# Optimization experiments

Measured on AMD Instinct MI355X. Metric: run time of the kernel, lower is better.

Reference implementation:

```python
import jax, jax.numpy as jnp
import numpy as np

FRACS = (0.25, 0.5, 0.25)  # per-expert top-fraction kept, from the original forward


def setup_inputs() -> dict:
    key = jax.random.key(0)
    ks = jax.random.split(key, 10)
    B, S, D, P, E, C = 1, 65536, 1024, 512, 3, 2
    s = 0.02
    return {
        "hidden_states": jax.random.normal(ks[0], (B, S, D), jnp.float32),
        "W_t1": jax.random.normal(ks[1], (D, P), jnp.float32) * s,   # TransMIL stand-in proj
        "W_cls1": jax.random.normal(ks[2], (P, C), jnp.float32) * s, # trans1 bag classifier
        "Wg0": jax.random.normal(ks[3], (P, 2), jnp.float32) * s,    # gate
        "Wg1": jax.random.normal(ks[4], (P, 2), jnp.float32) * s,    # gate1
        "Wg2": jax.random.normal(ks[5], (P, 2), jnp.float32) * s,    # gate2
        "W_clf": jax.random.normal(ks[6], (E, P, E), jnp.float32) * s,  # per-expert classifiers
        "W_a1": jax.random.normal(ks[7], (P, P), jnp.float32) * s,   # agg1 TransMIL stand-in proj
        "W_acls": jax.random.normal(ks[8], (P, C), jnp.float32) * s, # agg1 bag classifier
    }


def reference(hidden_states, W_t1, W_cls1, Wg0, Wg1, Wg2, W_clf, W_a1, W_acls):
    B, S, D = hidden_states.shape
    x = hidden_states.reshape(-1, D)               # (T, D) tokens
    T = x.shape[0]
    # trans1 (TransMIL stand-in): per-patch feature + mean-pool bag logits
    patches = jnp.tanh(x @ W_t1)                   # (T, P) patch_feature
    bag = patches.mean(0)
    Y_logits = (bag @ W_cls1)[None, :]             # (1, C)
    Y_prob = jax.nn.softmax(Y_logits, -1)
    Y_hat = jnp.argmax(Y_logits, -1)
    # three independent routers, softmax + top-1
    router_logits = patches @ Wg0                  # (T, 2)
    rw0 = jax.nn.softmax(router_logits.astype(jnp.float32), -1)
    w_top0 = rw0.max(-1)                           # top-1 routing weight (gate0) used as sort key for ALL experts
    sel0 = jnp.argmax(rw0, -1)
    sel1 = jnp.argmax(jax.nn.softmax((patches @ Wg1).astype(jnp.float32), -1), -1)
    sel2 = jnp.argmax(jax.nn.softmax((patches @ Wg2).astype(jnp.float32), -1), -1)
    masks = [sel0 == 1, sel1 == 1, sel2 == 1]      # expert_mask[e][1] token selection
    joint_losses = jnp.float32(0.0)
    sel_fs, nums_list = [], []
    for e in range(3):
        mask = masks[e]
        cnt = mask.sum().astype(jnp.int32)
        nums = jnp.floor(cnt.astype(jnp.float32) * FRACS[e]).astype(jnp.int32)
        nums = jnp.where(nums == 0, cnt, nums)     # 'if nums != 0 else all' branch
        key_ = jnp.where(mask, w_top0, -jnp.inf)
        order = jnp.argsort(-key_)                 # descending routing weight
        rank = jnp.zeros(T, jnp.int32).at[order].set(jnp.arange(T, dtype=jnp.int32))
        sel = mask & (rank < nums)                 # top-fraction tokens of this expert
        sel_f = sel.astype(patches.dtype)
        mean_feat = (patches * sel_f[:, None]).sum(0) / jnp.maximum(nums, 1).astype(patches.dtype)
        logits = mean_feat @ W_clf[e]              # (3,)
        if e < 2:                                  # CE loss only for experts 0,1
            joint_losses = joint_losses + (-jax.nn.log_softmax(logits)[e])
        sel_fs.append(sel_f)
        nums_list.append(nums)
    # agg1 (TransMIL stand-in) over concatenated represent_patchs == multiplicity-weighted mean
    feats2 = jnp.tanh(patches @ W_a1)              # (T, P)
    total_sel = sel_fs[0] + sel_fs[1] + sel_fs[2]
    total_n = (nums_list[0] + nums_list[1] + nums_list[2]).astype(patches.dtype)
    agg_bag = (feats2 * total_sel[:, None]).sum(0) / jnp.maximum(total_n, 1.0)
    e_Y_logits = (agg_bag @ W_acls)[None, :]
    e_Y_hat = jnp.argmax(e_Y_logits, -1)
    distribute = jnp.stack([jnp.asarray(T, jnp.int32), nums_list[0], nums_list[1], nums_list[2]])
    return (e_Y_logits, e_Y_hat, Y_logits, Y_prob, Y_hat, router_logits, joint_losses, distribute)
```

## Files before the change

### kernel.cpp

```cpp
#include <hip/hip_runtime.h>
#include <cstdint>
#include <cstddef>

#define T_TOK 65536
#define DDIM  1024
#define PDIM  512

typedef __attribute__((ext_vector_type(8))) short          shortx8;
typedef __attribute__((ext_vector_type(8))) unsigned short ushortx8;
typedef __attribute__((ext_vector_type(4))) float          floatx4;

__device__ __forceinline__ unsigned short f2bf_rn(float x){
  unsigned int u = __float_as_uint(x);
  unsigned int r = u + 0x7FFFu + ((u >> 16) & 1u);
  return (unsigned short)(r >> 16);
}
__device__ __forceinline__ float bf2f(unsigned short h){
  return __uint_as_float(((unsigned int)h) << 16);
}
__device__ __forceinline__ float ftanh(float x){
  float ez = __expf(2.f * x);
  return 1.f - 2.f / (ez + 1.f);
}

__global__ void prep(const float* __restrict__ Wt1, const float* __restrict__ Wa1,
                     unsigned short* __restrict__ W1th, unsigned short* __restrict__ W1tl,
                     unsigned short* __restrict__ Wath, unsigned short* __restrict__ Watl,
                     int* __restrict__ zbase)
{
  int gid = blockIdx.x * 256 + threadIdx.x;
  if (gid < 20544){ zbase[gid] = 0; return; }
  int i = gid - 20544;
  if (i < 524288){
    int p = i >> 10, k = i & 1023;
    float x = Wt1[(size_t)k * PDIM + p];
    unsigned short h = f2bf_rn(x);
    W1th[i] = h;
    W1tl[i] = f2bf_rn(x - bf2f(h));
    return;
  }
  i -= 524288;
  if (i < 262144){
    int n = i >> 9, k = i & 511;
    float x = Wa1[(size_t)k * PDIM + n];
    unsigned short h = f2bf_rn(x);
    Wath[i] = h;
    Watl[i] = f2bf_rn(x - bf2f(h));
  }
}

template<int MODE>
__global__ __launch_bounds__(256, 2)
void gemm_split(const float* __restrict__ A,
                const unsigned short* __restrict__ Bhg,
                const unsigned short* __restrict__ Blg,
                float* __restrict__ Cout,
                float* __restrict__ colacc,
                const int* __restrict__ cidx,
                const float* __restrict__ wgt,
                const int* __restrict__ params)
{
  constexpr int K = (MODE == 0) ? 1024 : 512;
  __shared__ unsigned short Ah[128][40];
  __shared__ unsigned short Al[128][40];
  __shared__ unsigned short Bh[128][40];
  __shared__ unsigned short Bl[128][40];
  __shared__ int   cidxl[128];
  __shared__ float wl[128];

  const int tid = threadIdx.x;
  const int m0 = blockIdx.y * 128;
  const int n0 = blockIdx.x * 128;

  if (MODE == 1){
    int count = params[21];
    if (m0 >= count) return;
    if (tid < 128){
      int g = m0 + tid;
      if (g < count){ cidxl[tid] = cidx[g]; wl[tid] = wgt[g]; }
      else          { cidxl[tid] = 0;       wl[tid] = 0.f;   }
    }
    __syncthreads();
  }

  const int lane = tid & 63;
  const int wv   = tid >> 6;
  const int wm   = (wv & 1) << 6;
  const int wn   = (wv >> 1) << 6;
  const int lr   = lane & 15;
  const int quad = lane >> 4;
  const int kb8  = quad << 3;

  floatx4 acc[4][4];
  #pragma unroll
  for (int i = 0; i < 4; i++)
    #pragma unroll
    for (int j = 0; j < 4; j++)
      acc[i][j] = (floatx4){0.f, 0.f, 0.f, 0.f};

  const int nkb = K >> 5;
  for (int kb = 0; kb < nkb; ++kb){
    const int k0 = kb << 5;
    #pragma unroll
    for (int i = 0; i < 4; i++){
      int lin = i * 256 + tid;
      int row = lin >> 3;
      int kq  = (lin & 7) << 2;
      size_t arow = (MODE == 0) ? (size_t)(m0 + row) : (size_t)cidxl[row];
      const float4 v = *(const float4*)(A + arow * K + k0 + kq);
      unsigned int ux = __float_as_uint(v.x), uy = __float_as_uint(v.y);
      unsigned int uz = __float_as_uint(v.z), uw = __float_as_uint(v.w);
      float rx = v.x - __uint_as_float(ux & 0xFFFF0000u);
      float ry = v.y - __uint_as_float(uy & 0xFFFF0000u);
      float rz = v.z - __uint_as_float(uz & 0xFFFF0000u);
      float rw = v.w - __uint_as_float(uw & 0xFFFF0000u);
      ushort4 h, l;
      h.x = (unsigned short)(ux >> 16); l.x = (unsigned short)(__float_as_uint(rx) >> 16);
      h.y = (unsigned short)(uy >> 16); l.y = (unsigned short)(__float_as_uint(ry) >> 16);
      h.z = (unsigned short)(uz >> 16); l.z = (unsigned short)(__float_as_uint(rz) >> 16);
      h.w = (unsigned short)(uw >> 16); l.w = (unsigned short)(__float_as_uint(rw) >> 16);
      *(ushort4*)&Ah[row][kq] = h;
      *(ushort4*)&Al[row][kq] = l;
    }
    #pragma unroll
    for (int i = 0; i < 2; i++){
      int lin = i * 256 + tid;
      int row = lin >> 2;
      int kq  = (lin & 3) << 3;
      size_t off = (size_t)(n0 + row) * K + k0 + kq;
      *(ushortx8*)&Bh[row][kq] = *(const ushortx8*)(Bhg + off);
      *(ushortx8*)&Bl[row][kq] = *(const ushortx8*)(Blg + off);
    }
    __syncthreads();
    shortx8 a0[4], a1[4], b0[4], b1[4];
    #pragma unroll
    for (int i = 0; i < 4; i++){
      a0[i] = *(const shortx8*)&Ah[wm + i * 16 + lr][kb8];
      a1[i] = *(const shortx8*)&Al[wm + i * 16 + lr][kb8];
      b0[i] = *(const shortx8*)&Bh[wn + i * 16 + lr][kb8];
      b1[i] = *(const shortx8*)&Bl[wn + i * 16 + lr][kb8];
    }
    #pragma unroll
    for (int i = 0; i < 4; i++){
      #pragma unroll
      for (int j = 0; j < 4; j++){
        acc[i][j] = __builtin_amdgcn_mfma_f32_16x16x32_bf16(a0[i], b0[j], acc[i][j], 0, 0, 0);
        acc[i][j] = __builtin_amdgcn_mfma_f32_16x16x32_bf16(a1[i], b0[j], acc[i][j], 0, 0, 0);
        acc[i][j] = __builtin_amdgcn_mfma_f32_16x16x32_bf16(a0[i], b1[j], acc[i][j], 0, 0, 0);
      }
    }
    __syncthreads();
  }

  float csum[4] = {0.f, 0.f, 0.f, 0.f};
  #pragma unroll
  for (int i = 0; i < 4; i++){
    float w0 = 1.f, w1 = 1.f, w2 = 1.f, w3 = 1.f;
    if (MODE == 1){
      const float4 wv4 = *(const float4*)&wl[wm + i * 16 + (quad << 2)];
      w0 = wv4.x; w1 = wv4.y; w2 = wv4.z; w3 = wv4.w;
    }
    #pragma unroll
    for (int j = 0; j < 4; j++){
      float t0 = ftanh(acc[i][j][0]);
      float t1 = ftanh(acc[i][j][1]);
      float t2 = ftanh(acc[i][j][2]);
      float t3 = ftanh(acc[i][j][3]);
      if (MODE == 0){
        size_t base = (size_t)(m0 + wm + i * 16 + (quad << 2)) * PDIM + (n0 + wn + j * 16 + lr);
        Cout[base]            = t0;
        Cout[base +     PDIM] = t1;
        Cout[base + 2 * PDIM] = t2;
        Cout[base + 3 * PDIM] = t3;
        csum[j] += t0 + t1 + t2 + t3;
      } else {
        csum[j] += t0 * w0 + t1 * w1 + t2 * w2 + t3 * w3;
      }
    }
  }
  #pragma unroll
  for (int j = 0; j < 4; j++){
    float s = csum[j];
    s += __shfl_xor(s, 16);
    s += __shfl_xor(s, 32);
    if (lane < 16) atomicAdd(&colacc[n0 + wn + j * 16 + lane], s);
  }
}

__global__ void gates_kernel(const float* __restrict__ patches,
                             const float* __restrict__ Wg0,
                             const float* __restrict__ Wg1,
                             const float* __restrict__ Wg2,
                             float* __restrict__ dout,
                             unsigned int* __restrict__ wkey,
                             unsigned char* __restrict__ mask3,
                             int* __restrict__ params,
                             int* __restrict__ hist)
{
  __shared__ int lc[3];
  const int tid = threadIdx.x;
  if (tid < 3) lc[tid] = 0;
  __syncthreads();
  const int lane = tid & 63;
  float wg[3][16];
  const float* Wgp[3] = {Wg0, Wg1, Wg2};
  #pragma unroll
  for (int g = 0; g < 3; g++){
    #pragma unroll
    for (int j = 0; j < 4; j++){
      float4 v = *(const float4*)(Wgp[g] + lane * 16 + j * 4);
      wg[g][j * 4 + 0] = v.x; wg[g][j * 4 + 1] = v.y;
      wg[g][j * 4 + 2] = v.z; wg[g][j * 4 + 3] = v.w;
    }
  }
  const int nw = gridDim.x << 2;
  for (int t = blockIdx.x * 4 + (tid >> 6); t < T_TOK; t += nw){
    const float* row = patches + (size_t)t * PDIM + lane * 8;
    float4 v0 = *(const float4*)row;
    float4 v1 = *(const float4*)(row + 4);
    float x[8] = {v0.x, v0.y, v0.z, v0.w, v1.x, v1.y, v1.z, v1.w};
    float g00 = 0, g01 = 0, g10 = 0, g11 = 0, g20 = 0, g21 = 0;
    #pragma unroll
    for (int j = 0; j < 8; j++){
      g00 += x[j] * wg[0][2 * j]; g01 += x[j] * wg[0][2 * j + 1];
      g10 += x[j] * wg[1][2 * j]; g11 += x[j] * wg[1][2 * j + 1];
      g20 += x[j] * wg[2][2 * j]; g21 += x[j] * wg[2][2 * j + 1];
    }
    #pragma unroll
    for (int off = 1; off < 64; off <<= 1){
      g00 += __shfl_xor(g00, off); g01 += __shfl_xor(g01, off);
      g10 += __shfl_xor(g10, off); g11 += __shfl_xor(g11, off);
      g20 += __shfl_xor(g20, off); g21 += __shfl_xor(g21, off);
    }
    if (lane == 0){
      dout[8 + 2 * t]     = g00;
      dout[8 + 2 * t + 1] = g01;
      int m0 = g01 > g00;
      int m1 = g11 > g10;
      int m2 = g21 > g20;
      mask3[t] = (unsigned char)(m0 | (m1 << 1) | (m2 << 2));
      float d = fabsf(g00 - g01);
      float w = 1.0f / (1.0f + __expf(-d));
      unsigned int u = __float_as_uint(w);
      u = u < 0x3F000000u ? 0x3F000000u : u;
      u = u > 0x3F7FFFFFu ? 0x3F7FFFFFu : u;
      wkey[t] = u;
      int b = (int)((u >> 11) & 0xFFFu);
      if (m0){ atomicAdd(&hist[b], 1);         atomicAdd(&lc[0], 1); }
      if (m1){ atomicAdd(&hist[4096 + b], 1);  atomicAdd(&lc[1], 1); }
      if (m2){ atomicAdd(&hist[8192 + b], 1);  atomicAdd(&lc[2], 1); }
    }
  }
  __syncthreads();
  if (tid < 3 && lc[tid]) atomicAdd(&params[tid], lc[tid]);
}

__global__ void find_bucket(int* __restrict__ params, const int* __restrict__ hist)
{
  __shared__ int cs[256], orig[256];
  __shared__ int selc, selrk;
  const int tid = threadIdx.x;
  for (int e = 0; e < 3; e++){
    int cnt = params[e];
    int shift = (e == 1) ? 1 : 2;
    int nums = cnt >> shift;
    if (nums == 0) nums = cnt;
    if (tid == 0) params[3 + e] = nums;
    __syncthreads();
    if (nums == 0){
      if (tid == 0){ params[6 + e] = -1; params[9 + e] = 0; }
      __syncthreads();
      continue;
    }
    const int* h = hist + e * 4096 + tid * 16;
    int s = 0;
    #pragma unroll
    for (int j = 0; j < 16; j++) s += h[j];
    cs[tid] = s; orig[tid] = s;
    __syncthreads();
    for (int off = 1; off < 256; off <<= 1){
      int v = (tid + off < 256) ? cs[tid + off] : 0;
      __syncthreads();
      cs[tid] += v;
      __syncthreads();
    }
    if (cs[tid] >= nums && (cs[tid] - orig[tid]) < nums){
      selc = tid; selrk = nums - (cs[tid] - orig[tid]);
    }
    __syncthreads();
    if (tid == 0){
      int ch = selc, rk = selrk;
      const int* hh = hist + e * 4096 + ch * 16;
      int acc = 0;
      for (int j = 15; j >= 0; j--){
        int c = hh[j];
        if (acc + c >= rk){ params[6 + e] = ch * 16 + j; params[9 + e] = rk - acc; break; }
        acc += c;
      }
    }
    __syncthreads();
  }
}

__global__ void level2hist(const int* __restrict__ params, const unsigned int* __restrict__ wkey,
                           const unsigned char* __restrict__ mask3, int* __restrict__ h2)
{
  const int e = blockIdx.y;
  const int B = params[6 + e];
  if (B < 0) return;
  const unsigned char bit = (unsigned char)(1u << e);
  const int t0 = blockIdx.x * 2048 + threadIdx.x;
  #pragma unroll
  for (int i = 0; i < 8; i++){
    int t = t0 + i * 256;
    if (mask3[t] & bit){
      unsigned int u = wkey[t];
      if ((int)((u >> 11) & 0xFFFu) == B) atomicAdd(&h2[e * 2048 + (u & 2047u)], 1);
    }
  }
}

__global__ void find_theta(int* __restrict__ params, const int* __restrict__ h2)
{
  const int e = blockIdx.x;
  const int tid = threadIdx.x;
  __shared__ int cs[256], orig[256];
  __shared__ int selc;
  int B = params[6 + e], rank = params[9 + e];
  if (B < 0){
    if (tid == 0){ params[12 + e] = (int)0xFFFFFFFFu; params[15 + e] = 0; params[18 + e] = 0; }
    return;
  }
  const int* h = h2 + e * 2048 + tid * 8;
  int s = 0;
  #pragma unroll
  for (int j = 0; j < 8; j++) s += h[j];
  cs[tid] = s; orig[tid] = s;
  __syncthreads();
  for (int off = 1; off < 256; off <<= 1){
    int v = (tid + off < 256) ? cs[tid + off] : 0;
    __syncthreads();
    cs[tid] += v;
    __syncthreads();
  }
  if (cs[tid] >= rank && (cs[tid] - orig[tid]) < rank) selc = tid;
  __syncthreads();
  if (tid == 0){
    int ch = selc;
    int rk = rank - (cs[ch] - orig[ch]);
    const int* hh = h2 + e * 2048 + ch * 8;
    int acc = 0;
    for (int j = 7; j >= 0; j--){
      int c = hh[j];
      if (acc + c >= rk){
        int sub = ch * 8 + j;
        params[12 + e] = (int)(0x3F000000u | ((unsigned)B << 11) | (unsigned)sub);
        params[15 + e] = rk - acc;
        params[18 + e] = c;
        break;
      }
      acc += c;
    }
  }
}

__global__ void mark_sel(const int* __restrict__ params, const unsigned int* __restrict__ wkey,
                         const unsigned char* __restrict__ mask3, unsigned char* __restrict__ selb)
{
  const int e = blockIdx.y;
  const int bx = blockIdx.x;
  const int tid = threadIdx.x;
  const unsigned int theta = (unsigned int)params[12 + e];
  const int r = params[15 + e];
  const int ceq = params[18 + e];
  const unsigned char bit = (unsigned char)(1u << e);
  unsigned char* sb = selb + e * T_TOK;
  if (ceq == r){
    int t0 = bx * 2048;
    #pragma unroll
    for (int i = 0; i < 8; i++){
      int t = t0 + i * 256 + tid;
      unsigned char mk = mask3[t] & bit;
      sb[t] = (mk && wkey[t] >= theta) ? 1 : 0;
    }
  } else {
    if (bx) return;
    __shared__ int basec;
    __shared__ int wsum[4];
    if (tid == 0) basec = 0;
    __syncthreads();
    const int lane = tid & 63, w = tid >> 6;
    for (int c = 0; c < 256; c++){
      int t = c * 256 + tid;
      unsigned char mk = mask3[t] & bit;
      unsigned int u = mk ? wkey[t] : 0u;
      bool gt = mk && (u > theta);
      bool eq = mk && (u == theta);
      unsigned long long bal = __ballot(eq);
      if (lane == 0) wsum[w] = __popcll(bal);
      __syncthreads();
      int wbase = 0;
      for (int ww = 0; ww < w; ww++) wbase += wsum[ww];
      int pos = basec + wbase + __popcll(bal & ((1ull << lane) - 1ull));
      sb[t] = (gt || (eq && pos < r)) ? 1 : 0;
      __syncthreads();
      if (tid == 0) basec += wsum[0] + wsum[1] + wsum[2] + wsum[3];
      __syncthreads();
    }
  }
}

__global__ void compact(const unsigned char* __restrict__ selb, int* __restrict__ cidx,
                        float* __restrict__ wgt, int* __restrict__ params)
{
  int t = blockIdx.x * 256 + threadIdx.x;
  int ts = selb[t] + selb[T_TOK + t] + selb[2 * T_TOK + t];
  int lane = threadIdx.x & 63;
  unsigned long long bal = __ballot(ts > 0);
  int base = 0;
  if (lane == 0) base = atomicAdd(&params[21], __popcll(bal));
  base = __shfl(base, 0);
  if (ts){
    int pos = base + __popcll(bal & ((1ull << lane) - 1ull));
    cidx[pos] = t;
    wgt[pos] = (float)ts;
  }
}

__global__ void meanfeat_c(const float* __restrict__ patches, const unsigned char* __restrict__ selb,
                           const int* __restrict__ cidx, const int* __restrict__ params,
                           float* __restrict__ mf)
{
  const int count = params[21];
  const int base = blockIdx.x * 256;
  if (base >= count) return;
  const int n = min(256, count - base);
  const int tid = threadIdx.x;
  __shared__ int cl[256];
  __shared__ unsigned char f0s[256], f1s[256];
  if (tid < n){
    int c = cidx[base + tid];
    cl[tid] = c;
    f0s[tid] = selb[c];
    f1s[tid] = selb[T_TOK + c];
  }
  __syncthreads();
  float s00 = 0, s01 = 0, s10 = 0, s11 = 0;
  for (int i = 0; i < n; i++){
    int f0 = f0s[i], f1 = f1s[i];
    if (f0 | f1){
      float2 v = *(const float2*)(patches + (size_t)cl[i] * PDIM + tid * 2);
      if (f0){ s00 += v.x; s01 += v.y; }
      if (f1){ s10 += v.x; s11 += v.y; }
    }
  }
  atomicAdd(&mf[tid * 2],       s00);
  atomicAdd(&mf[tid * 2 + 1],   s01);
  atomicAdd(&mf[512 + tid * 2],     s10);
  atomicAdd(&mf[512 + tid * 2 + 1], s11);
}

__global__ void finalize(const float* __restrict__ bagsum, const float* __restrict__ aggsum,
                         const float* __restrict__ mf, const int* __restrict__ params,
                         const float* __restrict__ Wcls1, const float* __restrict__ Wclf,
                         const float* __restrict__ Wacls, float* __restrict__ dout)
{
  const int lane = threadIdx.x;
  const int nums0 = params[3], nums1 = params[4], nums2 = params[5];
  const float invT = 1.0f / 65536.0f;
  const float inv0 = 1.0f / (float)(nums0 > 0 ? nums0 : 1);
  const float inv1 = 1.0f / (float)(nums1 > 0 ? nums1 : 1);
  const float totn = (float)(nums0 + nums1 + nums2);
  const float invA = 1.0f / fmaxf(totn, 1.0f);
  float y0 = 0, y1 = 0, a0 = 0, a1 = 0;
  float l00 = 0, l01 = 0, l02 = 0, l10 = 0, l11 = 0, l12 = 0;
  #pragma unroll
  for (int j = 0; j < 8; j++){
    int p = lane * 8 + j;
    float bg = bagsum[p] * invT;
    y0 += bg * Wcls1[p * 2]; y1 += bg * Wcls1[p * 2 + 1];
    float ag = aggsum[p] * invA;
    a0 += ag * Wacls[p * 2]; a1 += ag * Wacls[p * 2 + 1];
    float m0v = mf[p] * inv0;
    l00 += m0v * Wclf[p * 3]; l01 += m0v * Wclf[p * 3 + 1]; l02 += m0v * Wclf[p * 3 + 2];
    float m1v = mf[512 + p] * inv1;
    l10 += m1v * Wclf[1536 + p * 3]; l11 += m1v * Wclf[1536 + p * 3 + 1]; l12 += m1v * Wclf[1536 + p * 3 + 2];
  }
  #pragma unroll
  for (int off = 1; off < 64; off <<= 1){
    y0 += __shfl_xor(y0, off);   y1 += __shfl_xor(y1, off);
    a0 += __shfl_xor(a0, off);   a1 += __shfl_xor(a1, off);
    l00 += __shfl_xor(l00, off); l01 += __shfl_xor(l01, off); l02 += __shfl_xor(l02, off);
    l10 += __shfl_xor(l10, off); l11 += __shfl_xor(l11, off); l12 += __shfl_xor(l12, off);
  }
  if (lane == 0){
    dout[0] = a0; dout[1] = a1;
    dout[2] = (a1 > a0) ? 1.0f : 0.0f;
    dout[3] = y0; dout[4] = y1;
    float mx = fmaxf(y0, y1), e0 = expf(y0 - mx), e1 = expf(y1 - mx), inv = 1.0f / (e0 + e1);
    dout[5] = e0 * inv; dout[6] = e1 * inv;
    dout[7] = (y1 > y0) ? 1.0f : 0.0f;
    float m3 = fmaxf(fmaxf(l00, l01), l02);
    float lse0 = m3 + logf(expf(l00 - m3) + expf(l01 - m3) + expf(l02 - m3));
    float m4 = fmaxf(fmaxf(l10, l11), l12);
    float lse1 = m4 + logf(expf(l10 - m4) + expf(l11 - m4) + expf(l12 - m4));
    dout[131080] = (lse0 - l00) + (lse1 - l11);
    dout[131081] = 65536.0f;
    dout[131082] = (float)nums0;
    dout[131083] = (float)nums1;
    dout[131084] = (float)nums2;
  }
}

extern "C" void kernel_launch(void* const* d_in, const int* in_sizes, int n_in,
                              void* d_out, int out_size, void* d_ws, size_t ws_size,
                              hipStream_t stream)
{
  const float* X      = (const float*)d_in[0];
  const float* W_t1   = (const float*)d_in[1];
  const float* W_cls1 = (const float*)d_in[2];
  const float* Wg0    = (const float*)d_in[3];
  const float* Wg1    = (const float*)d_in[4];
  const float* Wg2    = (const float*)d_in[5];
  const float* W_clf  = (const float*)d_in[6];
  const float* W_a1   = (const float*)d_in[7];
  const float* W_acls = (const float*)d_in[8];
  float* dout = (float*)d_out;
  char* ws = (char*)d_ws;

  float*          patches = (float*)         (ws + 0);
  unsigned short* W1th    = (unsigned short*)(ws + 134217728);
  unsigned short* W1tl    = (unsigned short*)(ws + 135266304);
  unsigned short* Wath    = (unsigned short*)(ws + 136314880);
  unsigned short* Watl    = (unsigned short*)(ws + 136839168);
  unsigned int*   wkey    = (unsigned int*)  (ws + 137363456);
  unsigned char*  mask3   = (unsigned char*) (ws + 137625600);
  unsigned char*  selb    = (unsigned char*) (ws + 137691136);
  int*            cidx    = (int*)           (ws + 137887744);
  float*          wgt     = (float*)         (ws + 138149888);
  int*            zbase   = (int*)           (ws + 138412032);
  int*            hist    = zbase;
  int*            h2      = zbase + 12288;
  int*            params  = zbase + 18432;
  float*          bagsum  = (float*)(zbase + 18496);
  float*          aggsum  = (float*)(zbase + 19008);
  float*          mf      = (float*)(zbase + 19520);

  prep<<<3153, 256, 0, stream>>>(W_t1, W_a1, W1th, W1tl, Wath, Watl, zbase);

  gemm_split<0><<<dim3(4, 512), 256, 0, stream>>>(
      X, W1th, W1tl, patches, bagsum, nullptr, nullptr, nullptr);

  gates_kernel<<<512, 256, 0, stream>>>(
      patches, Wg0, Wg1, Wg2, dout, wkey, mask3, params, hist);

  find_bucket<<<1, 256, 0, stream>>>(params, hist);
  level2hist<<<dim3(32, 3), 256, 0, stream>>>(params, wkey, mask3, h2);
  find_theta<<<3, 256, 0, stream>>>(params, h2);
  mark_sel<<<dim3(32, 3), 256, 0, stream>>>(params, wkey, mask3, selb);
  compact<<<256, 256, 0, stream>>>(selb, cidx, wgt, params);

  meanfeat_c<<<256, 256, 0, stream>>>(patches, selb, cidx, params, mf);

  gemm_split<1><<<dim3(4, 512), 256, 0, stream>>>(
      patches, Wath, Watl, nullptr, aggsum, cidx, wgt, params);

  finalize<<<1, 64, 0, stream>>>(bagsum, aggsum, mf, params, W_cls1, W_clf, W_acls, dout);
}
```

Measured before the change: 732.6 us.

## Rewrite split-bf16 GEMM with 256x256 tiles, double-buffered LDS and direct-to-LDS weight loads

Both split-precision GEMMs now use 256x256 tiles with 512 threads, double-buffered LDS and direct global-to-LDS loads for the weights. The weights are pre-swizzled in prep into a tiled, XOR-permuted layout to avoid bank conflicts. The k-loop is split into four MFMA phases with explicit waitcnt, barriers and setprio so the next tile's loads overlap the current tile's compute, and mode 0 blocks are remapped for L2 locality. The larger tiles cut re-reads of A and B from global memory. In exchange the kernel uses more LDS and registers per block, and the hand-placed waits and barriers are fragile.

```diff
diff --git a/kernel.cpp b/kernel.cpp
--- a/kernel.cpp
+++ b/kernel.cpp
@@ -23,6 +23,34 @@
   return 1.f - 2.f / (ez + 1.f);
 }
 
+__device__ __forceinline__ void gload16(const void* g, void* l){
+  __builtin_amdgcn_global_load_lds(
+      (const __attribute__((address_space(1))) unsigned int*)g,
+      (__attribute__((address_space(3))) unsigned int*)l, 16, 0, 0);
+}
+__device__ __forceinline__ void bar(){
+  asm volatile("" ::: "memory");
+  __builtin_amdgcn_s_barrier();
+  asm volatile("" ::: "memory");
+}
+#define WAIT_VMC(n) asm volatile("s_waitcnt vmcnt(" #n ")" ::: "memory")
+#define WAIT_LGKM0  do { asm volatile("s_waitcnt lgkmcnt(0)" ::: "memory"); \
+                         __builtin_amdgcn_sched_barrier(0); } while(0)
+
+__device__ __forceinline__ void split2(const float4 a, const float4 b,
+                                       ushortx8* hi, ushortx8* lo){
+  float vs[8] = {a.x, a.y, a.z, a.w, b.x, b.y, b.z, b.w};
+  ushortx8 h, l;
+  #pragma unroll
+  for (int j = 0; j < 8; j++){
+    unsigned int u = __float_as_uint(vs[j]);
+    float r = vs[j] - __uint_as_float(u & 0xFFFF0000u);
+    h[j] = (unsigned short)(u >> 16);
+    l[j] = (unsigned short)(__float_as_uint(r) >> 16);
+  }
+  *hi = h; *lo = l;
+}
+
 __global__ void prep(const float* __restrict__ Wt1, const float* __restrict__ Wa1,
                      unsigned short* __restrict__ W1th, unsigned short* __restrict__ W1tl,
                      unsigned short* __restrict__ Wath, unsigned short* __restrict__ Watl,
@@ -32,8 +60,15 @@
   if (gid < 20544){ zbase[gid] = 0; return; }
   int i = gid - 20544;
   if (i < 524288){
-    int p = i >> 10, k = i & 1023;
-    float x = Wt1[(size_t)k * PDIM + p];
+    int e   = i & 7;
+    int g16 = i >> 3;
+    int s   = g16 & 3;
+    int row = (g16 >> 2) & 255;
+    int tb  = g16 >> 10;
+    int nb  = tb & 1, kt = tb >> 1;
+    int n = nb * 256 + row;
+    int k = kt * 32 + ((s ^ (row & 3)) << 3) + e;
+    float x = Wt1[(size_t)k * PDIM + n];
     unsigned short h = f2bf_rn(x);
     W1th[i] = h;
     W1tl[i] = f2bf_rn(x - bf2f(h));
@@ -41,7 +76,14 @@
   }
   i -= 524288;
   if (i < 262144){
-    int n = i >> 9, k = i & 511;
+    int e   = i & 7;
+    int g16 = i >> 3;
+    int s   = g16 & 3;
+    int row = (g16 >> 2) & 255;
+    int tb  = g16 >> 10;
+    int nb  = tb & 1, kt = tb >> 1;
+    int n = nb * 256 + row;
+    int k = kt * 32 + ((s ^ (row & 3)) << 3) + e;
     float x = Wa1[(size_t)k * PDIM + n];
     unsigned short h = f2bf_rn(x);
     Wath[i] = h;
@@ -50,7 +92,7 @@
 }
 
 template<int MODE>
-__global__ __launch_bounds__(256, 2)
+__global__ __launch_bounds__(512, 2)
 void gemm_split(const float* __restrict__ A,
                 const unsigned short* __restrict__ Bhg,
                 const unsigned short* __restrict__ Blg,
@@ -60,22 +102,26 @@
                 const float* __restrict__ wgt,
                 const int* __restrict__ params)
 {
-  constexpr int K = (MODE == 0) ? 1024 : 512;
-  __shared__ unsigned short Ah[128][40];
-  __shared__ unsigned short Al[128][40];
-  __shared__ unsigned short Bh[128][40];
-  __shared__ unsigned short Bl[128][40];
-  __shared__ int   cidxl[128];
-  __shared__ float wl[128];
+  constexpr int K  = (MODE == 0) ? 1024 : 512;
+  constexpr int NT = K >> 5;
+
+  __shared__ unsigned short AhL[2][8192];
+  __shared__ unsigned short AlL[2][8192];
+  __shared__ unsigned short BhL[2][8192];
+  __shared__ unsigned short BlL[2][8192];
+  __shared__ int   cidxl[256];
+  __shared__ float wl[256];
 
   const int tid = threadIdx.x;
-  const int m0 = blockIdx.y * 128;
-  const int n0 = blockIdx.x * 128;
+  const int d = blockIdx.x + (blockIdx.y << 1);
+  const int lin = (MODE == 0) ? (((d & 7) << 6) + (d >> 3)) : d;
+  const int bx = lin & 1, by = lin >> 1;
+  const int m0 = by << 8, n0 = bx << 8;
 
   if (MODE == 1){
-    int count = params[21];
+    const int count = params[21];
     if (m0 >= count) return;
-    if (tid < 128){
+    if (tid < 256){
       int g = m0 + tid;
       if (g < count){ cidxl[tid] = cidx[g]; wl[tid] = wgt[g]; }
       else          { cidxl[tid] = 0;       wl[tid] = 0.f;   }
@@ -85,105 +131,198 @@
 
   const int lane = tid & 63;
   const int wv   = tid >> 6;
-  const int wm   = (wv & 1) << 6;
-  const int wn   = (wv >> 1) << 6;
-  const int lr   = lane & 15;
-  const int quad = lane >> 4;
-  const int kb8  = quad << 3;
-
-  floatx4 acc[4][4];
-  #pragma unroll
-  for (int i = 0; i < 4; i++)
+  const int wm   = wv >> 2;
+  const int wn   = wv & 3;
+  const int lr   = lane & 15, quad = lane >> 4;
+  const int sq   = (quad ^ (lr & 3)) << 4;
+
+  const int abase = (wm * 128 + lr) * 64 + sq;
+  const int bbase = (wn * 64  + lr) * 64 + sq;
+
+  const int rowW = tid >> 1, half = tid & 1;
+  const size_t arowg = (MODE == 0) ? (size_t)(m0 + rowW) : (size_t)cidxl[rowW];
+  const float* ap = A + arowg * K + half * 16;
+  const int wb0 = rowW * 64 + ((( half * 2     ) ^ (rowW & 3)) << 4);
+  const int wb1 = rowW * 64 + ((( half * 2 + 1 ) ^ (rowW & 3)) << 4);
+
+  floatx4 acc[8][4];
+  #pragma unroll
+  for (int i = 0; i < 8; i++)
     #pragma unroll
     for (int j = 0; j < 4; j++)
       acc[i][j] = (floatx4){0.f, 0.f, 0.f, 0.f};
 
-  const int nkb = K >> 5;
-  for (int kb = 0; kb < nkb; ++kb){
-    const int k0 = kb << 5;
-    #pragma unroll
-    for (int i = 0; i < 4; i++){
-      int lin = i * 256 + tid;
-      int row = lin >> 3;
-      int kq  = (lin & 7) << 2;
-      size_t arow = (MODE == 0) ? (size_t)(m0 + row) : (size_t)cidxl[row];
-      const float4 v = *(const float4*)(A + arow * K + k0 + kq);
-      unsigned int ux = __float_as_uint(v.x), uy = __float_as_uint(v.y);
-      unsigned int uz = __float_as_uint(v.z), uw = __float_as_uint(v.w);
-      float rx = v.x - __uint_as_float(ux & 0xFFFF0000u);
-      float ry = v.y - __uint_as_float(uy & 0xFFFF0000u);
-      float rz = v.z - __uint_as_float(uz & 0xFFFF0000u);
-      float rw = v.w - __uint_as_float(uw & 0xFFFF0000u);
-      ushort4 h, l;
-      h.x = (unsigned short)(ux >> 16); l.x = (unsigned short)(__float_as_uint(rx) >> 16);
-      h.y = (unsigned short)(uy >> 16); l.y = (unsigned short)(__float_as_uint(ry) >> 16);
-      h.z = (unsigned short)(uz >> 16); l.z = (unsigned short)(__float_as_uint(rz) >> 16);
-      h.w = (unsigned short)(uw >> 16); l.w = (unsigned short)(__float_as_uint(rw) >> 16);
-      *(ushort4*)&Ah[row][kq] = h;
-      *(ushort4*)&Al[row][kq] = l;
-    }
-    #pragma unroll
-    for (int i = 0; i < 2; i++){
-      int lin = i * 256 + tid;
-      int row = lin >> 2;
-      int kq  = (lin & 3) << 3;
-      size_t off = (size_t)(n0 + row) * K + k0 + kq;
-      *(ushortx8*)&Bh[row][kq] = *(const ushortx8*)(Bhg + off);
-      *(ushortx8*)&Bl[row][kq] = *(const ushortx8*)(Blg + off);
-    }
-    __syncthreads();
-    shortx8 a0[4], a1[4], b0[4], b1[4];
-    #pragma unroll
-    for (int i = 0; i < 4; i++){
-      a0[i] = *(const shortx8*)&Ah[wm + i * 16 + lr][kb8];
-      a1[i] = *(const shortx8*)&Al[wm + i * 16 + lr][kb8];
-      b0[i] = *(const shortx8*)&Bh[wn + i * 16 + lr][kb8];
-      b1[i] = *(const shortx8*)&Bl[wn + i * 16 + lr][kb8];
-    }
-    #pragma unroll
-    for (int i = 0; i < 4; i++){
+  float4 av0, av1, av2, av3;
+
+  {
+    av0 = *(const float4*)(ap + 0);
+    av1 = *(const float4*)(ap + 4);
+    av2 = *(const float4*)(ap + 8);
+    av3 = *(const float4*)(ap + 12);
+    const size_t tb = (size_t)bx * 8192;
+    gload16(Bhg + tb + tid * 8,        (char*)BhL[0] + tid * 16);
+    gload16(Bhg + tb + 4096 + tid * 8, (char*)BhL[0] + 8192 + tid * 16);
+    gload16(Blg + tb + tid * 8,        (char*)BlL[0] + tid * 16);
+    gload16(Blg + tb + 4096 + tid * 8, (char*)BlL[0] + 8192 + tid * 16);
+    WAIT_VMC(4);
+    ushortx8 h, l;
+    split2(av0, av1, &h, &l);
+    *(ushortx8*)((char*)AhL[0] + wb0) = h;
+    *(ushortx8*)((char*)AlL[0] + wb0) = l;
+    split2(av2, av3, &h, &l);
+    *(ushortx8*)((char*)AhL[0] + wb1) = h;
+    *(ushortx8*)((char*)AlL[0] + wb1) = l;
+    WAIT_VMC(0);
+    asm volatile("s_waitcnt lgkmcnt(0)" ::: "memory");
+    bar();
+  }
+
+  #pragma unroll 2
+  for (int t = 0; t < NT; ++t){
+    const int cur = t & 1, nxt = cur ^ 1;
+    const int kn = (t + 1 < NT) ? (t + 1) : t;
+    const char* AhC = (const char*)AhL[cur];
+    const char* AlC = (const char*)AlL[cur];
+    const char* BhC = (const char*)BhL[cur];
+    const char* BlC = (const char*)BlL[cur];
+
+    shortx8 aH[4], aL[4], bH0[2], bL0[2], bH1[2], bL1[2];
+
+    #pragma unroll
+    for (int mt = 0; mt < 4; mt++){
+      aH[mt] = *(const shortx8*)(AhC + abase + mt * 1024);
+      aL[mt] = *(const shortx8*)(AlC + abase + mt * 1024);
+    }
+    #pragma unroll
+    for (int nt = 0; nt < 2; nt++){
+      bH0[nt] = *(const shortx8*)(BhC + bbase + nt * 1024);
+      bL0[nt] = *(const shortx8*)(BlC + bbase + nt * 1024);
+    }
+    {
+      const float* apk = ap + kn * 32;
+      av0 = *(const float4*)(apk);
+      av1 = *(const float4*)(apk + 4);
+      av2 = *(const float4*)(apk + 8);
+      av3 = *(const float4*)(apk + 12);
+    }
+    bar();
+    WAIT_LGKM0;
+    __builtin_amdgcn_s_setprio(1);
+    #pragma unroll
+    for (int mt = 0; mt < 4; mt++)
       #pragma unroll
-      for (int j = 0; j < 4; j++){
-        acc[i][j] = __builtin_amdgcn_mfma_f32_16x16x32_bf16(a0[i], b0[j], acc[i][j], 0, 0, 0);
-        acc[i][j] = __builtin_amdgcn_mfma_f32_16x16x32_bf16(a1[i], b0[j], acc[i][j], 0, 0, 0);
-        acc[i][j] = __builtin_amdgcn_mfma_f32_16x16x32_bf16(a0[i], b1[j], acc[i][j], 0, 0, 0);
+      for (int nt = 0; nt < 2; nt++){
+        acc[mt][nt] = __builtin_amdgcn_mfma_f32_16x16x32_bf16(aH[mt], bH0[nt], acc[mt][nt], 0, 0, 0);
+        acc[mt][nt] = __builtin_amdgcn_mfma_f32_16x16x32_bf16(aL[mt], bH0[nt], acc[mt][nt], 0, 0, 0);
+        acc[mt][nt] = __builtin_amdgcn_mfma_f32_16x16x32_bf16(aH[mt], bL0[nt], acc[mt][nt], 0, 0, 0);
       }
-    }
-    __syncthreads();
+    __builtin_amdgcn_s_setprio(0);
+    bar();
+
+    #pragma unroll
+    for (int nt = 0; nt < 2; nt++){
+      bH1[nt] = *(const shortx8*)(BhC + bbase + (2 + nt) * 1024);
+      bL1[nt] = *(const shortx8*)(BlC + bbase + (2 + nt) * 1024);
+    }
+    {
+      const size_t tb = (size_t)(kn * 2 + bx) * 8192;
+      gload16(Bhg + tb + tid * 8,        (char*)BhL[nxt] + tid * 16);
+      gload16(Bhg + tb + 4096 + tid * 8, (char*)BhL[nxt] + 8192 + tid * 16);
+      gload16(Blg + tb + tid * 8,        (char*)BlL[nxt] + tid * 16);
+      gload16(Blg + tb + 4096 + tid * 8, (char*)BlL[nxt] + 8192 + tid * 16);
+    }
+    bar();
+    WAIT_LGKM0;
+    __builtin_amdgcn_s_setprio(1);
+    #pragma unroll
+    for (int mt = 0; mt < 4; mt++)
+      #pragma unroll
+      for (int nt = 0; nt < 2; nt++){
+        acc[mt][2 + nt] = __builtin_amdgcn_mfma_f32_16x16x32_bf16(aH[mt], bH1[nt], acc[mt][2 + nt], 0, 0, 0);
+        acc[mt][2 + nt] = __builtin_amdgcn_mfma_f32_16x16x32_bf16(aL[mt], bH1[nt], acc[mt][2 + nt], 0, 0, 0);
+        acc[mt][2 + nt] = __builtin_amdgcn_mfma_f32_16x16x32_bf16(aH[mt], bL1[nt], acc[mt][2 + nt], 0, 0, 0);
+      }
+    __builtin_amdgcn_s_setprio(0);
+    bar();
+
+    #pragma unroll
+    for (int mt = 0; mt < 4; mt++){
+      aH[mt] = *(const shortx8*)(AhC + abase + (4 + mt) * 1024);
+      aL[mt] = *(const shortx8*)(AlC + abase + (4 + mt) * 1024);
+    }
+    WAIT_VMC(4);
+    {
+      ushortx8 h, l;
+      split2(av0, av1, &h, &l);
+      *(ushortx8*)((char*)AhL[nxt] + wb0) = h;
+      *(ushortx8*)((char*)AlL[nxt] + wb0) = l;
+      split2(av2, av3, &h, &l);
+      *(ushortx8*)((char*)AhL[nxt] + wb1) = h;
+      *(ushortx8*)((char*)AlL[nxt] + wb1) = l;
+    }
+    bar();
+    WAIT_LGKM0;
+    __builtin_amdgcn_s_setprio(1);
+    #pragma unroll
+    for (int mt = 0; mt < 4; mt++)
+      #pragma unroll
+      for (int nt = 0; nt < 2; nt++){
+        acc[4 + mt][nt] = __builtin_amdgcn_mfma_f32_16x16x32_bf16(aH[mt], bH0[nt], acc[4 + mt][nt], 0, 0, 0);
+        acc[4 + mt][nt] = __builtin_amdgcn_mfma_f32_16x16x32_bf16(aL[mt], bH0[nt], acc[4 + mt][nt], 0, 0, 0);
+        acc[4 + mt][nt] = __builtin_amdgcn_mfma_f32_16x16x32_bf16(aH[mt], bL0[nt], acc[4 + mt][nt], 0, 0, 0);
+      }
+    __builtin_amdgcn_s_setprio(0);
+    bar();
+
+    WAIT_VMC(0);
+    bar();
+    WAIT_LGKM0;
+    __builtin_amdgcn_s_setprio(1);
+    #pragma unroll
+    for (int mt = 0; mt < 4; mt++)
+      #pragma unroll
+      for (int nt = 0; nt < 2; nt++){
+        acc[4 + mt][2 + nt] = __builtin_amdgcn_mfma_f32_16x16x32_bf16(aH[mt], bH1[nt], acc[4 + mt][2 + nt], 0, 0, 0);
+        acc[4 + mt][2 + nt] = __builtin_amdgcn_mfma_f32_16x16x32_bf16(aL[mt], bH1[nt], acc[4 + mt][2 + nt], 0, 0, 0);
+        acc[4 + mt][2 + nt] = __builtin_amdgcn_mfma_f32_16x16x32_bf16(aH[mt], bL1[nt], acc[4 + mt][2 + nt], 0, 0, 0);
+      }
+    __builtin_amdgcn_s_setprio(0);
+    bar();
   }
 
   float csum[4] = {0.f, 0.f, 0.f, 0.f};
   #pragma unroll
-  for (int i = 0; i < 4; i++){
+  for (int mt = 0; mt < 8; mt++){
     float w0 = 1.f, w1 = 1.f, w2 = 1.f, w3 = 1.f;
     if (MODE == 1){
-      const float4 wv4 = *(const float4*)&wl[wm + i * 16 + (quad << 2)];
+      const float4 wv4 = *(const float4*)&wl[wm * 128 + mt * 16 + (quad << 2)];
       w0 = wv4.x; w1 = wv4.y; w2 = wv4.z; w3 = wv4.w;
     }
     #pragma unroll
-    for (int j = 0; j < 4; j++){
-      float t0 = ftanh(acc[i][j][0]);
-      float t1 = ftanh(acc[i][j][1]);
-      float t2 = ftanh(acc[i][j][2]);
-      float t3 = ftanh(acc[i][j][3]);
+    for (int nt = 0; nt < 4; nt++){
+      float t0 = ftanh(acc[mt][nt][0]);
+      float t1 = ftanh(acc[mt][nt][1]);
+      float t2 = ftanh(acc[mt][nt][2]);
+      float t3 = ftanh(acc[mt][nt][3]);
       if (MODE == 0){
-        size_t base = (size_t)(m0 + wm + i * 16 + (quad << 2)) * PDIM + (n0 + wn + j * 16 + lr);
+        size_t base = (size_t)(m0 + wm * 128 + mt * 16 + (quad << 2)) * PDIM
+                    + (n0 + wn * 64 + nt * 16 + lr);
         Cout[base]            = t0;
         Cout[base +     PDIM] = t1;
         Cout[base + 2 * PDIM] = t2;
         Cout[base + 3 * PDIM] = t3;
-        csum[j] += t0 + t1 + t2 + t3;
+        csum[nt] += t0 + t1 + t2 + t3;
       } else {
-        csum[j] += t0 * w0 + t1 * w1 + t2 * w2 + t3 * w3;
+        csum[nt] += t0 * w0 + t1 * w1 + t2 * w2 + t3 * w3;
       }
     }
   }
   #pragma unroll
-  for (int j = 0; j < 4; j++){
-    float s = csum[j];
+  for (int nt = 0; nt < 4; nt++){
+    float s = csum[nt];
     s += __shfl_xor(s, 16);
     s += __shfl_xor(s, 32);
-    if (lane < 16) atomicAdd(&colacc[n0 + wn + j * 16 + lane], s);
+    if (lane < 16) atomicAdd(&colacc[n0 + wn * 64 + nt * 16 + lane], s);
   }
 }
 
@@ -548,7 +687,7 @@
 
   prep<<<3153, 256, 0, stream>>>(W_t1, W_a1, W1th, W1tl, Wath, Watl, zbase);
 
-  gemm_split<0><<<dim3(4, 512), 256, 0, stream>>>(
+  gemm_split<0><<<dim3(2, 256), 512, 0, stream>>>(
       X, W1th, W1tl, patches, bagsum, nullptr, nullptr, nullptr);
 
   gates_kernel<<<512, 256, 0, stream>>>(
@@ -562,7 +701,7 @@
 
   meanfeat_c<<<256, 256, 0, stream>>>(patches, selb, cidx, params, mf);
 
-  gemm_split<1><<<dim3(4, 512), 256, 0, stream>>>(
+  gemm_split<1><<<dim3(2, 256), 512, 0, stream>>>(
       patches, Wath, Watl, nullptr, aggsum, cidx, wgt, params);
 
   finalize<<<1, 64, 0, stream>>>(bagsum, aggsum, mf, params, W_cls1, W_clf, W_acls, dout);
```

Result: slower. 765.8 us (+4.5%).

## Drop LDS staging in split-bf16 GEMM using MFMA-fragment-ordered weights and register prefetch

Applied to the files above, without the earlier changes.

The prep kernel now writes the bf16 hi/lo weight copies in the exact per-lane MFMA fragment order. This lets the GEMM load B fragments straight from global memory and load A rows directly into registers, with no shared-memory staging and no __syncthreads. A two-stage register double buffer prefetches the next K tile while the current one is split and multiplied. MODE 0 also remaps block IDs so that blocks sharing A rows land on the same XCD. Separately, the gates_kernel grid grows from 512 to 2048 blocks, and meanfeat_c moves to 128-token chunks with twice as many blocks. The trade-off is that each wave now does uncoalesced-looking direct global loads of A rows, with no reuse through LDS across waves in a block.

```diff
diff --git a/kernel.cpp b/kernel.cpp
--- a/kernel.cpp
+++ b/kernel.cpp
@@ -32,8 +32,14 @@
   if (gid < 20544){ zbase[gid] = 0; return; }
   int i = gid - 20544;
   if (i < 524288){
-    int p = i >> 10, k = i & 1023;
-    float x = Wt1[(size_t)k * PDIM + p];
+    int e    = i & 7;
+    int lane = (i >> 3) & 63;
+    int j    = (i >> 9) & 7;
+    int kt   = (i >> 12) & 31;
+    int bx   = (i >> 17) & 3;
+    int n = bx * 128 + ((j >> 2) << 6) + ((j & 3) << 4) + (lane & 15);
+    int k = kt * 32 + ((lane >> 4) << 3) + e;
+    float x = Wt1[(size_t)k * PDIM + n];
     unsigned short h = f2bf_rn(x);
     W1th[i] = h;
     W1tl[i] = f2bf_rn(x - bf2f(h));
@@ -41,7 +47,13 @@
   }
   i -= 524288;
   if (i < 262144){
-    int n = i >> 9, k = i & 511;
+    int e    = i & 7;
+    int lane = (i >> 3) & 63;
+    int j    = (i >> 9) & 7;
+    int kt   = (i >> 12) & 15;
+    int bx   = (i >> 16) & 3;
+    int n = bx * 128 + ((j >> 2) << 6) + ((j & 3) << 4) + (lane & 15);
+    int k = kt * 32 + ((lane >> 4) << 3) + e;
     float x = Wa1[(size_t)k * PDIM + n];
     unsigned short h = f2bf_rn(x);
     Wath[i] = h;
@@ -60,20 +72,27 @@
                 const float* __restrict__ wgt,
                 const int* __restrict__ params)
 {
-  constexpr int K = (MODE == 0) ? 1024 : 512;
-  __shared__ unsigned short Ah[128][40];
-  __shared__ unsigned short Al[128][40];
-  __shared__ unsigned short Bh[128][40];
-  __shared__ unsigned short Bl[128][40];
+  constexpr int K   = (MODE == 0) ? 1024 : 512;
+  constexpr int NKT = K >> 5;
+
   __shared__ int   cidxl[128];
   __shared__ float wl[128];
 
   const int tid = threadIdx.x;
-  const int m0 = blockIdx.y * 128;
-  const int n0 = blockIdx.x * 128;
+  const int d = blockIdx.x + (blockIdx.y << 2);
+  int bx, by;
+  if (MODE == 0){
+    const int xcd = d & 7, m = d >> 3;
+    bx = m & 3;
+    by = xcd + ((m >> 2) << 3);
+  } else {
+    bx = blockIdx.x;
+    by = blockIdx.y;
+  }
+  const int m0 = by << 7, n0 = bx << 7;
 
   if (MODE == 1){
-    int count = params[21];
+    const int count = params[21];
     if (m0 >= count) return;
     if (tid < 128){
       int g = m0 + tid;
@@ -85,11 +104,21 @@
 
   const int lane = tid & 63;
   const int wv   = tid >> 6;
-  const int wm   = (wv & 1) << 6;
-  const int wn   = (wv >> 1) << 6;
-  const int lr   = lane & 15;
-  const int quad = lane >> 4;
-  const int kb8  = quad << 3;
+  const int wm   = wv >> 1;
+  const int wn   = wv & 1;
+  const int lr   = lane & 15, quad = lane >> 4;
+
+  const float* apt[4];
+  #pragma unroll
+  for (int mt = 0; mt < 4; mt++){
+    int rloc = wm * 64 + mt * 16 + lr;
+    size_t row = (MODE == 0) ? (size_t)(m0 + rloc) : (size_t)cidxl[rloc];
+    apt[mt] = A + row * K + (quad << 3);
+  }
+  const char* bhp = (const char*)Bhg
+      + ((size_t)(bx * NKT) * 8 + wn * 4) * 1024 + lane * 16;
+  const char* blp = (const char*)Blg
+      + ((size_t)(bx * NKT) * 8 + wn * 4) * 1024 + lane * 16;
 
   floatx4 acc[4][4];
   #pragma unroll
@@ -98,92 +127,113 @@
     for (int j = 0; j < 4; j++)
       acc[i][j] = (floatx4){0.f, 0.f, 0.f, 0.f};
 
-  const int nkb = K >> 5;
-  for (int kb = 0; kb < nkb; ++kb){
-    const int k0 = kb << 5;
-    #pragma unroll
-    for (int i = 0; i < 4; i++){
-      int lin = i * 256 + tid;
-      int row = lin >> 3;
-      int kq  = (lin & 7) << 2;
-      size_t arow = (MODE == 0) ? (size_t)(m0 + row) : (size_t)cidxl[row];
-      const float4 v = *(const float4*)(A + arow * K + k0 + kq);
-      unsigned int ux = __float_as_uint(v.x), uy = __float_as_uint(v.y);
-      unsigned int uz = __float_as_uint(v.z), uw = __float_as_uint(v.w);
-      float rx = v.x - __uint_as_float(ux & 0xFFFF0000u);
-      float ry = v.y - __uint_as_float(uy & 0xFFFF0000u);
-      float rz = v.z - __uint_as_float(uz & 0xFFFF0000u);
-      float rw = v.w - __uint_as_float(uw & 0xFFFF0000u);
-      ushort4 h, l;
-      h.x = (unsigned short)(ux >> 16); l.x = (unsigned short)(__float_as_uint(rx) >> 16);
-      h.y = (unsigned short)(uy >> 16); l.y = (unsigned short)(__float_as_uint(ry) >> 16);
-      h.z = (unsigned short)(uz >> 16); l.z = (unsigned short)(__float_as_uint(rz) >> 16);
-      h.w = (unsigned short)(uw >> 16); l.w = (unsigned short)(__float_as_uint(rw) >> 16);
-      *(ushort4*)&Ah[row][kq] = h;
-      *(ushort4*)&Al[row][kq] = l;
-    }
-    #pragma unroll
-    for (int i = 0; i < 2; i++){
-      int lin = i * 256 + tid;
-      int row = lin >> 2;
-      int kq  = (lin & 3) << 3;
-      size_t off = (size_t)(n0 + row) * K + k0 + kq;
-      *(ushortx8*)&Bh[row][kq] = *(const ushortx8*)(Bhg + off);
-      *(ushortx8*)&Bl[row][kq] = *(const ushortx8*)(Blg + off);
-    }
-    __syncthreads();
-    shortx8 a0[4], a1[4], b0[4], b1[4];
-    #pragma unroll
-    for (int i = 0; i < 4; i++){
-      a0[i] = *(const shortx8*)&Ah[wm + i * 16 + lr][kb8];
-      a1[i] = *(const shortx8*)&Al[wm + i * 16 + lr][kb8];
-      b0[i] = *(const shortx8*)&Bh[wn + i * 16 + lr][kb8];
-      b1[i] = *(const shortx8*)&Bl[wn + i * 16 + lr][kb8];
-    }
-    #pragma unroll
-    for (int i = 0; i < 4; i++){
-      #pragma unroll
-      for (int j = 0; j < 4; j++){
-        acc[i][j] = __builtin_amdgcn_mfma_f32_16x16x32_bf16(a0[i], b0[j], acc[i][j], 0, 0, 0);
-        acc[i][j] = __builtin_amdgcn_mfma_f32_16x16x32_bf16(a1[i], b0[j], acc[i][j], 0, 0, 0);
-        acc[i][j] = __builtin_amdgcn_mfma_f32_16x16x32_bf16(a0[i], b1[j], acc[i][j], 0, 0, 0);
-      }
-    }
-    __syncthreads();
-  }
+  float4  a0[4][2], a1[4][2];
+  shortx8 bv[8];
+
+#define LOADA(dst, ktv)                                                   \
+  _Pragma("unroll")                                                       \
+  for (int mt = 0; mt < 4; mt++){                                         \
+    dst[mt][0] = *(const float4*)(apt[mt] + (ktv) * 32);                  \
+    dst[mt][1] = *(const float4*)(apt[mt] + (ktv) * 32 + 4);              \
+  }
+
+#define LOADB(ktv)                                                        \
+  {                                                                       \
+    const char* _bh = bhp + (size_t)(ktv) * 8192;                         \
+    const char* _bl = blp + (size_t)(ktv) * 8192;                         \
+    _Pragma("unroll")                                                     \
+    for (int nt = 0; nt < 4; nt++){                                       \
+      bv[nt]     = *(const shortx8*)(_bh + nt * 1024);                    \
+      bv[4 + nt] = *(const shortx8*)(_bl + nt * 1024);                    \
+    }                                                                     \
+  }
+
+#define GSTEP(av)                                                         \
+  {                                                                       \
+    shortx8 aH[4], aL[4];                                                 \
+    _Pragma("unroll")                                                     \
+    for (int mt = 0; mt < 4; mt++){                                       \
+      const float4 v0 = av[mt][0], v1 = av[mt][1];                        \
+      float vs[8] = {v0.x, v0.y, v0.z, v0.w, v1.x, v1.y, v1.z, v1.w};     \
+      ushortx8 h, l;                                                      \
+      _Pragma("unroll")                                                   \
+      for (int e = 0; e < 8; e++){                                        \
+        unsigned int u = __float_as_uint(vs[e]);                          \
+        float r = vs[e] - __uint_as_float(u & 0xFFFF0000u);               \
+        h[e] = (unsigned short)(u >> 16);                                 \
+        l[e] = (unsigned short)(__float_as_uint(r) >> 16);                \
+      }                                                                   \
+      aH[mt] = *(shortx8*)&h; aL[mt] = *(shortx8*)&l;                     \
+    }                                                                     \
+    _Pragma("unroll")                                                     \
+    for (int mt = 0; mt < 4; mt++)                                        \
+      _Pragma("unroll")                                                   \
+      for (int nt = 0; nt < 4; nt++)                                      \
+        acc[mt][nt] = __builtin_amdgcn_mfma_f32_16x16x32_bf16(            \
+            aH[mt], bv[nt], acc[mt][nt], 0, 0, 0);                        \
+    _Pragma("unroll")                                                     \
+    for (int mt = 0; mt < 4; mt++)                                        \
+      _Pragma("unroll")                                                   \
+      for (int nt = 0; nt < 4; nt++)                                      \
+        acc[mt][nt] = __builtin_amdgcn_mfma_f32_16x16x32_bf16(            \
+            aL[mt], bv[nt], acc[mt][nt], 0, 0, 0);                        \
+    _Pragma("unroll")                                                     \
+    for (int mt = 0; mt < 4; mt++)                                        \
+      _Pragma("unroll")                                                   \
+      for (int nt = 0; nt < 4; nt++)                                      \
+        acc[mt][nt] = __builtin_amdgcn_mfma_f32_16x16x32_bf16(            \
+            aH[mt], bv[4 + nt], acc[mt][nt], 0, 0, 0);                    \
+  }
+
+  LOADA(a0, 0);
+  for (int t = 0; t < NKT; t += 2){
+    const int t1 = (t + 1 < NKT) ? t + 1 : NKT - 1;
+    const int t2 = (t + 2 < NKT) ? t + 2 : NKT - 1;
+    LOADB(t);
+    LOADA(a1, t1);
+    GSTEP(a0);
+    LOADB(t1);
+    LOADA(a0, t2);
+    GSTEP(a1);
+  }
+
+#undef LOADA
+#undef LOADB
+#undef GSTEP
 
   float csum[4] = {0.f, 0.f, 0.f, 0.f};
   #pragma unroll
-  for (int i = 0; i < 4; i++){
+  for (int mt = 0; mt < 4; mt++){
     float w0 = 1.f, w1 = 1.f, w2 = 1.f, w3 = 1.f;
     if (MODE == 1){
-      const float4 wv4 = *(const float4*)&wl[wm + i * 16 + (quad << 2)];
+      const float4 wv4 = *(const float4*)&wl[wm * 64 + mt * 16 + (quad << 2)];
       w0 = wv4.x; w1 = wv4.y; w2 = wv4.z; w3 = wv4.w;
     }
     #pragma unroll
-    for (int j = 0; j < 4; j++){
-      float t0 = ftanh(acc[i][j][0]);
-      float t1 = ftanh(acc[i][j][1]);
-      float t2 = ftanh(acc[i][j][2]);
-      float t3 = ftanh(acc[i][j][3]);
+    for (int nt = 0; nt < 4; nt++){
+      float t0 = ftanh(acc[mt][nt][0]);
+      float t1 = ftanh(acc[mt][nt][1]);
+      float t2 = ftanh(acc[mt][nt][2]);
+      float t3 = ftanh(acc[mt][nt][3]);
       if (MODE == 0){
-        size_t base = (size_t)(m0 + wm + i * 16 + (quad << 2)) * PDIM + (n0 + wn + j * 16 + lr);
+        size_t base = (size_t)(m0 + wm * 64 + mt * 16 + (quad << 2)) * PDIM
+                    + (n0 + wn * 64 + nt * 16 + lr);
         Cout[base]            = t0;
         Cout[base +     PDIM] = t1;
         Cout[base + 2 * PDIM] = t2;
         Cout[base + 3 * PDIM] = t3;
-        csum[j] += t0 + t1 + t2 + t3;
+        csum[nt] += t0 + t1 + t2 + t3;
       } else {
-        csum[j] += t0 * w0 + t1 * w1 + t2 * w2 + t3 * w3;
+        csum[nt] += t0 * w0 + t1 * w1 + t2 * w2 + t3 * w3;
       }
     }
   }
   #pragma unroll
-  for (int j = 0; j < 4; j++){
-    float s = csum[j];
+  for (int nt = 0; nt < 4; nt++){
+    float s = csum[nt];
     s += __shfl_xor(s, 16);
     s += __shfl_xor(s, 32);
-    if (lane < 16) atomicAdd(&colacc[n0 + wn + j * 16 + lane], s);
+    if (lane < 16) atomicAdd(&colacc[n0 + wn * 64 + nt * 16 + lane], s);
   }
 }
 
@@ -432,12 +482,12 @@
                            float* __restrict__ mf)
 {
   const int count = params[21];
-  const int base = blockIdx.x * 256;
+  const int base = blockIdx.x * 128;
   if (base >= count) return;
-  const int n = min(256, count - base);
+  const int n = min(128, count - base);
   const int tid = threadIdx.x;
-  __shared__ int cl[256];
-  __shared__ unsigned char f0s[256], f1s[256];
+  __shared__ int cl[128];
+  __shared__ unsigned char f0s[128], f1s[128];
   if (tid < n){
     int c = cidx[base + tid];
     cl[tid] = c;
@@ -551,7 +601,7 @@
   gemm_split<0><<<dim3(4, 512), 256, 0, stream>>>(
       X, W1th, W1tl, patches, bagsum, nullptr, nullptr, nullptr);
 
-  gates_kernel<<<512, 256, 0, stream>>>(
+  gates_kernel<<<2048, 256, 0, stream>>>(
       patches, Wg0, Wg1, Wg2, dout, wkey, mask3, params, hist);
 
   find_bucket<<<1, 256, 0, stream>>>(params, hist);
@@ -560,7 +610,7 @@
   mark_sel<<<dim3(32, 3), 256, 0, stream>>>(params, wkey, mask3, selb);
   compact<<<256, 256, 0, stream>>>(selb, cidx, wgt, params);
 
-  meanfeat_c<<<256, 256, 0, stream>>>(patches, selb, cidx, params, mf);
+  meanfeat_c<<<512, 256, 0, stream>>>(patches, selb, cidx, params, mf);
 
   gemm_split<1><<<dim3(4, 512), 256, 0, stream>>>(
       patches, Wath, Watl, nullptr, aggsum, cidx, wgt, params);
```

After: 853.3 us. +16.5%, slower.
